# Kernel optimization log

Measured on AMD Instinct MI355X. Metric: run time of the kernel, lower is better.

## Reference

```python
import jax, jax.numpy as jnp
import numpy as np

N, E = 100000, 1600000
NODE_DIM, EDGE_DIM, HID = 128, 64, 128

def _mlp(x, w1, b1, w2, b2):
    # 2-layer MLP: Linear -> ReLU -> Linear (weights stored torch-style [out,in])
    return jax.nn.relu(x @ w1.T + b1) @ w2.T + b2

def setup_inputs() -> dict:
    key = jax.random.key(0)
    ks = jax.random.split(key, 24)
    g = lambda k, shp, fan: jax.random.normal(k, shp, jnp.float32) * (1.0 / np.sqrt(fan))
    return {
        "x": jax.random.normal(ks[0], (N, NODE_DIM), jnp.float32),
        "pos": jax.random.normal(ks[1], (N, 3), jnp.float32),
        "edge_index": jax.random.randint(ks[2], (2, E), 0, N),
        "edge_attr": jax.random.normal(ks[3], (E, EDGE_DIM), jnp.float32),
        # node_net: MLP(node_dim -> hid -> hid)
        "node_w1": g(ks[4], (HID, NODE_DIM), NODE_DIM), "node_b1": jnp.zeros((HID,), jnp.float32),
        "node_w2": g(ks[5], (HID, HID), HID), "node_b2": jnp.zeros((HID,), jnp.float32),
        # edge_net: MLP(edge_dim -> hid -> hid)
        "edge_w1": g(ks[6], (HID, EDGE_DIM), EDGE_DIM), "edge_b1": jnp.zeros((HID,), jnp.float32),
        "edge_w2": g(ks[7], (HID, HID), HID), "edge_b2": jnp.zeros((HID,), jnp.float32),
        # msg_net: Linear(hid, hid)
        "msg_w": g(ks[8], (HID, HID), HID), "msg_b": jnp.zeros((HID,), jnp.float32),
        # gate: MLP(edge_dim + node_dim -> hid -> hid)
        "gate_w1": g(ks[9], (HID, EDGE_DIM + NODE_DIM), EDGE_DIM + NODE_DIM), "gate_b1": jnp.zeros((HID,), jnp.float32),
        "gate_w2": g(ks[10], (HID, HID), HID), "gate_b2": jnp.zeros((HID,), jnp.float32),
        # centroid_lin: Linear(node_dim, hid)
        "cent_w": g(ks[11], (HID, NODE_DIM), NODE_DIM), "cent_b": jnp.zeros((HID,), jnp.float32),
        # layer norm
        "ln_g": jnp.ones((HID,), jnp.float32), "ln_b": jnp.zeros((HID,), jnp.float32),
        # out_transform: Linear(hid, node_dim)
        "out_w": g(ks[12], (NODE_DIM, HID), HID), "out_b": jnp.zeros((NODE_DIM,), jnp.float32),
    }

def reference(x, pos, edge_index, edge_attr,
              node_w1, node_b1, node_w2, node_b2,
              edge_w1, edge_b1, edge_w2, edge_b2,
              msg_w, msg_b,
              gate_w1, gate_b1, gate_w2, gate_b2,
              cent_w, cent_b, ln_g, ln_b, out_w, out_b):
    row, col = edge_index[0], edge_index[1]
    h_node = _mlp(x, node_w1, node_b1, node_w2, node_b2)          # (N, HID)
    h_edge = _mlp(edge_attr, edge_w1, edge_b1, edge_w2, edge_b2)   # (E, HID)
    msg_j = (h_edge * h_node[col]) @ msg_w.T + msg_b               # (E, HID)
    gate = _mlp(jnp.concatenate([edge_attr, x[col]], axis=-1),
                gate_w1, gate_b1, gate_w2, gate_b2)                # (E, HID)
    msg_j = msg_j * jax.nn.sigmoid(gate)
    aggr = jax.ops.segment_sum(msg_j, row, num_segments=x.shape[0])  # (N, HID)
    out = (x @ cent_w.T + cent_b) + aggr
    mu = jnp.mean(out, axis=-1, keepdims=True)
    var = jnp.var(out, axis=-1, keepdims=True)
    out = (out - mu) * jax.lax.rsqrt(var + 1e-5) * ln_g + ln_b
    return jax.nn.relu(out) @ out_w.T + out_b                      # (N, NODE_DIM)
```

## Files before the change

### kernel.cpp

```cpp
#include <hip/hip_runtime.h>

#define NN 100000
#define NE 1600000

typedef __bf16 bf16;
typedef bf16 bf16x8 __attribute__((ext_vector_type(8)));
typedef bf16 bf16x4 __attribute__((ext_vector_type(4)));
typedef float f32x4 __attribute__((ext_vector_type(4)));

__device__ __forceinline__ f32x4 mfma16(bf16x8 a, bf16x8 b, f32x4 c) {
    return __builtin_amdgcn_mfma_f32_16x16x32_bf16(a, b, c, 0, 0, 0);
}

__global__ void cvt_kernel(const float* __restrict__ s, bf16* __restrict__ d, int n4) {
    int i = blockIdx.x * 256 + threadIdx.x;
    if (i < n4) {
        f32x4 v = ((const f32x4*)s)[i];
        bf16x4 o;
        o[0] = (bf16)v[0]; o[1] = (bf16)v[1]; o[2] = (bf16)v[2]; o[3] = (bf16)v[3];
        ((bf16x4*)d)[i] = o;
    }
}

__launch_bounds__(256, 3)
__global__ void node_kernel(const bf16* __restrict__ xb,
                            const bf16* __restrict__ w1, const float* __restrict__ b1,
                            const bf16* __restrict__ w2, const float* __restrict__ b2,
                            const bf16* __restrict__ wc, const float* __restrict__ bc,
                            const bf16* __restrict__ wg1,
                            float* __restrict__ h_node, float* __restrict__ cent,
                            float* __restrict__ gx) {
    const int S = 136;
    __shared__ __align__(16) bf16 sX[64 * S];
    __shared__ __align__(16) bf16 sH[64 * S];
    const int tid = threadIdx.x;
    const int m0 = blockIdx.x * 64;
    {
        int e = tid >> 2, p = tid & 3;
        int gm = m0 + e;
        uint4 z = {0, 0, 0, 0};
        uint4* dst = (uint4*)(sX + e * S + p * 32);
        if (gm < NN) {
            const uint4* src = (const uint4*)(xb + (size_t)gm * 128 + p * 32);
#pragma unroll
            for (int j = 0; j < 4; ++j) dst[j] = src[j];
        } else {
#pragma unroll
            for (int j = 0; j < 4; ++j) dst[j] = z;
        }
    }
    __syncthreads();
    const int lane = tid & 63, wave = tid >> 6, t16 = lane & 15, quad = lane >> 4;
    const int n0 = wave * 32, koff = quad * 8;
    const f32x4 z4 = {0.f, 0.f, 0.f, 0.f};
    f32x4 acc[4][2];

#pragma unroll
    for (int mt = 0; mt < 4; ++mt) { acc[mt][0] = z4; acc[mt][1] = z4; }
#pragma unroll
    for (int ks = 0; ks < 4; ++ks) {
        bf16x8 bb0 = *(const bf16x8*)(w1 + (n0 + t16) * 128 + ks * 32 + koff);
        bf16x8 bb1 = *(const bf16x8*)(w1 + (n0 + 16 + t16) * 128 + ks * 32 + koff);
#pragma unroll
        for (int mt = 0; mt < 4; ++mt) {
            bf16x8 a = *(const bf16x8*)(sX + (mt * 16 + t16) * S + ks * 32 + koff);
            acc[mt][0] = mfma16(a, bb0, acc[mt][0]);
            acc[mt][1] = mfma16(a, bb1, acc[mt][1]);
        }
    }
    {
        float bi0 = b1[n0 + t16], bi1 = b1[n0 + 16 + t16];
#pragma unroll
        for (int mt = 0; mt < 4; ++mt)
#pragma unroll
            for (int nt = 0; nt < 2; ++nt) {
                int n = n0 + nt * 16 + t16;
                float bb = nt ? bi1 : bi0;
#pragma unroll
                for (int r = 0; r < 4; ++r) {
                    float v = acc[mt][nt][r] + bb;
                    sH[(mt * 16 + quad * 4 + r) * S + n] = (bf16)(v > 0.f ? v : 0.f);
                }
            }
    }
    __syncthreads();

#pragma unroll
    for (int mt = 0; mt < 4; ++mt) { acc[mt][0] = z4; acc[mt][1] = z4; }
#pragma unroll
    for (int ks = 0; ks < 4; ++ks) {
        bf16x8 bb0 = *(const bf16x8*)(w2 + (n0 + t16) * 128 + ks * 32 + koff);
        bf16x8 bb1 = *(const bf16x8*)(w2 + (n0 + 16 + t16) * 128 + ks * 32 + koff);
#pragma unroll
        for (int mt = 0; mt < 4; ++mt) {
            bf16x8 a = *(const bf16x8*)(sH + (mt * 16 + t16) * S + ks * 32 + koff);
            acc[mt][0] = mfma16(a, bb0, acc[mt][0]);
            acc[mt][1] = mfma16(a, bb1, acc[mt][1]);
        }
    }
    {
        float bi0 = b2[n0 + t16], bi1 = b2[n0 + 16 + t16];
#pragma unroll
        for (int mt = 0; mt < 4; ++mt)
#pragma unroll
            for (int nt = 0; nt < 2; ++nt) {
                int n = n0 + nt * 16 + t16;
                float bb = nt ? bi1 : bi0;
#pragma unroll
                for (int r = 0; r < 4; ++r) {
                    int gm = m0 + mt * 16 + quad * 4 + r;
                    if (gm < NN) h_node[(size_t)gm * 128 + n] = acc[mt][nt][r] + bb;
                }
            }
    }

#pragma unroll
    for (int mt = 0; mt < 4; ++mt) { acc[mt][0] = z4; acc[mt][1] = z4; }
#pragma unroll
    for (int ks = 0; ks < 4; ++ks) {
        bf16x8 bb0 = *(const bf16x8*)(wc + (n0 + t16) * 128 + ks * 32 + koff);
        bf16x8 bb1 = *(const bf16x8*)(wc + (n0 + 16 + t16) * 128 + ks * 32 + koff);
#pragma unroll
        for (int mt = 0; mt < 4; ++mt) {
            bf16x8 a = *(const bf16x8*)(sX + (mt * 16 + t16) * S + ks * 32 + koff);
            acc[mt][0] = mfma16(a, bb0, acc[mt][0]);
            acc[mt][1] = mfma16(a, bb1, acc[mt][1]);
        }
    }
    {
        float bi0 = bc[n0 + t16], bi1 = bc[n0 + 16 + t16];
#pragma unroll
        for (int mt = 0; mt < 4; ++mt)
#pragma unroll
            for (int nt = 0; nt < 2; ++nt) {
                int n = n0 + nt * 16 + t16;
                float bb = nt ? bi1 : bi0;
#pragma unroll
                for (int r = 0; r < 4; ++r) {
                    int gm = m0 + mt * 16 + quad * 4 + r;
                    if (gm < NN) cent[(size_t)gm * 128 + n] = acc[mt][nt][r] + bb;
                }
            }
    }

#pragma unroll
    for (int mt = 0; mt < 4; ++mt) { acc[mt][0] = z4; acc[mt][1] = z4; }
#pragma unroll
    for (int ks = 0; ks < 4; ++ks) {
        bf16x8 bb0 = *(const bf16x8*)(wg1 + (n0 + t16) * 192 + 64 + ks * 32 + koff);
        bf16x8 bb1 = *(const bf16x8*)(wg1 + (n0 + 16 + t16) * 192 + 64 + ks * 32 + koff);
#pragma unroll
        for (int mt = 0; mt < 4; ++mt) {
            bf16x8 a = *(const bf16x8*)(sX + (mt * 16 + t16) * S + ks * 32 + koff);
            acc[mt][0] = mfma16(a, bb0, acc[mt][0]);
            acc[mt][1] = mfma16(a, bb1, acc[mt][1]);
        }
    }
#pragma unroll
    for (int mt = 0; mt < 4; ++mt)
#pragma unroll
        for (int nt = 0; nt < 2; ++nt) {
            int n = n0 + nt * 16 + t16;
#pragma unroll
            for (int r = 0; r < 4; ++r) {
                int gm = m0 + mt * 16 + quad * 4 + r;
                if (gm < NN) gx[(size_t)gm * 128 + n] = acc[mt][nt][r];
            }
        }
}

__launch_bounds__(256, 3)
__global__ void edge_kernel(const float* __restrict__ edge_attr,
                            const int* __restrict__ erow, const int* __restrict__ ecol,
                            const float* __restrict__ hnode, const float* __restrict__ gx,
                            const bf16* __restrict__ we1, const float* __restrict__ be1,
                            const bf16* __restrict__ we2, const float* __restrict__ be2,
                            const bf16* __restrict__ wm, const float* __restrict__ bm,
                            const bf16* __restrict__ wg1, const float* __restrict__ bg1,
                            const bf16* __restrict__ wg2, const float* __restrict__ bg2,
                            float* __restrict__ aggr) {
    const int SE = 72, S = 136;
    __shared__ __align__(16) bf16 sEA[64 * SE];
    __shared__ __align__(16) bf16 sT[64 * S];
    __shared__ __align__(16) bf16 sX[64 * S];
    __shared__ int rowS[64], colS[64];
    const int tid = threadIdx.x;
    const int e0 = blockIdx.x * 64;
    if (tid < 64) { rowS[tid] = erow[e0 + tid]; colS[tid] = ecol[e0 + tid]; }
#pragma unroll
    for (int i = 0; i < 4; ++i) {
        int idx = tid * 4 + i * 1024;
        int e = idx >> 6, k = idx & 63;
        f32x4 v = *(const f32x4*)(edge_attr + (size_t)(e0 + e) * 64 + k);
        bf16x4 o;
        o[0] = (bf16)v[0]; o[1] = (bf16)v[1]; o[2] = (bf16)v[2]; o[3] = (bf16)v[3];
        *(bf16x4*)(sEA + e * SE + k) = o;
    }
    __syncthreads();
    const int lane = tid & 63, wave = tid >> 6, t16 = lane & 15, quad = lane >> 4;
    const int n0 = wave * 32, koff = quad * 8;
    const f32x4 z4 = {0.f, 0.f, 0.f, 0.f};
    f32x4 acc[4][2];

    float gval[4][2][4];
#pragma unroll
    for (int mt = 0; mt < 4; ++mt)
#pragma unroll
        for (int r = 0; r < 4; ++r) {
            const float* grow = gx + (size_t)colS[mt * 16 + quad * 4 + r] * 128;
            gval[mt][0][r] = grow[n0 + t16];
            gval[mt][1][r] = grow[n0 + 16 + t16];
        }

#pragma unroll
    for (int mt = 0; mt < 4; ++mt) { acc[mt][0] = z4; acc[mt][1] = z4; }
#pragma unroll
    for (int ks = 0; ks < 2; ++ks) {
        bf16x8 bb0 = *(const bf16x8*)(wg1 + (n0 + t16) * 192 + ks * 32 + koff);
        bf16x8 bb1 = *(const bf16x8*)(wg1 + (n0 + 16 + t16) * 192 + ks * 32 + koff);
#pragma unroll
        for (int mt = 0; mt < 4; ++mt) {
            bf16x8 a = *(const bf16x8*)(sEA + (mt * 16 + t16) * SE + ks * 32 + koff);
            acc[mt][0] = mfma16(a, bb0, acc[mt][0]);
            acc[mt][1] = mfma16(a, bb1, acc[mt][1]);
        }
    }
    {
        float bi0 = bg1[n0 + t16], bi1 = bg1[n0 + 16 + t16];
#pragma unroll
        for (int mt = 0; mt < 4; ++mt)
#pragma unroll
            for (int nt = 0; nt < 2; ++nt) {
                int n = n0 + nt * 16 + t16;
                float bb = nt ? bi1 : bi0;
#pragma unroll
                for (int r = 0; r < 4; ++r) {
                    float v = acc[mt][nt][r] + bb + gval[mt][nt][r];
                    sT[(mt * 16 + quad * 4 + r) * S + n] = (bf16)(v > 0.f ? v : 0.f);
                }
            }
    }
    __syncthreads();

    f32x4 gsig[4][2];
#pragma unroll
    for (int mt = 0; mt < 4; ++mt) { gsig[mt][0] = z4; gsig[mt][1] = z4; acc[mt][0] = z4; acc[mt][1] = z4; }
#pragma unroll
    for (int ks = 0; ks < 4; ++ks) {
        bf16x8 bb0 = *(const bf16x8*)(wg2 + (n0 + t16) * 128 + ks * 32 + koff);
        bf16x8 bb1 = *(const bf16x8*)(wg2 + (n0 + 16 + t16) * 128 + ks * 32 + koff);
#pragma unroll
        for (int mt = 0; mt < 4; ++mt) {
            bf16x8 a = *(const bf16x8*)(sT + (mt * 16 + t16) * S + ks * 32 + koff);
            gsig[mt][0] = mfma16(a, bb0, gsig[mt][0]);
            gsig[mt][1] = mfma16(a, bb1, gsig[mt][1]);
        }
    }
#pragma unroll
    for (int ks = 0; ks < 2; ++ks) {
        bf16x8 bb0 = *(const bf16x8*)(we1 + (n0 + t16) * 64 + ks * 32 + koff);
        bf16x8 bb1 = *(const bf16x8*)(we1 + (n0 + 16 + t16) * 64 + ks * 32 + koff);
#pragma unroll
        for (int mt = 0; mt < 4; ++mt) {
            bf16x8 a = *(const bf16x8*)(sEA + (mt * 16 + t16) * SE + ks * 32 + koff);
            acc[mt][0] = mfma16(a, bb0, acc[mt][0]);
            acc[mt][1] = mfma16(a, bb1, acc[mt][1]);
        }
    }
    {
        float bi0 = bg2[n0 + t16], bi1 = bg2[n0 + 16 + t16];
#pragma unroll
        for (int mt = 0; mt < 4; ++mt)
#pragma unroll
            for (int nt = 0; nt < 2; ++nt) {
                float bb = nt ? bi1 : bi0;
#pragma unroll
                for (int r = 0; r < 4; ++r) {
                    float v = gsig[mt][nt][r] + bb;
                    gsig[mt][nt][r] = 1.f / (1.f + __expf(-v));
                }
            }
    }
    {
        float bi0 = be1[n0 + t16], bi1 = be1[n0 + 16 + t16];
#pragma unroll
        for (int mt = 0; mt < 4; ++mt)
#pragma unroll
            for (int nt = 0; nt < 2; ++nt) {
                int n = n0 + nt * 16 + t16;
                float bb = nt ? bi1 : bi0;
#pragma unroll
                for (int r = 0; r < 4; ++r) {
                    float v = acc[mt][nt][r] + bb;
                    sX[(mt * 16 + quad * 4 + r) * S + n] = (bf16)(v > 0.f ? v : 0.f);
                }
            }
    }
    __syncthreads();

    float hval[4][2][4];
#pragma unroll
    for (int mt = 0; mt < 4; ++mt)
#pragma unroll
        for (int r = 0; r < 4; ++r) {
            const float* h = hnode + (size_t)colS[mt * 16 + quad * 4 + r] * 128;
            hval[mt][0][r] = h[n0 + t16];
            hval[mt][1][r] = h[n0 + 16 + t16];
        }

#pragma unroll
    for (int mt = 0; mt < 4; ++mt) { acc[mt][0] = z4; acc[mt][1] = z4; }
#pragma unroll
    for (int ks = 0; ks < 4; ++ks) {
        bf16x8 bb0 = *(const bf16x8*)(we2 + (n0 + t16) * 128 + ks * 32 + koff);
        bf16x8 bb1 = *(const bf16x8*)(we2 + (n0 + 16 + t16) * 128 + ks * 32 + koff);
#pragma unroll
        for (int mt = 0; mt < 4; ++mt) {
            bf16x8 a = *(const bf16x8*)(sX + (mt * 16 + t16) * S + ks * 32 + koff);
            acc[mt][0] = mfma16(a, bb0, acc[mt][0]);
            acc[mt][1] = mfma16(a, bb1, acc[mt][1]);
        }
    }
    {
        float bi0 = be2[n0 + t16], bi1 = be2[n0 + 16 + t16];
#pragma unroll
        for (int mt = 0; mt < 4; ++mt)
#pragma unroll
            for (int nt = 0; nt < 2; ++nt) {
                float bb = nt ? bi1 : bi0;
#pragma unroll
                for (int r = 0; r < 4; ++r)
                    acc[mt][nt][r] = (acc[mt][nt][r] + bb) * hval[mt][nt][r];
            }
    }
    __syncthreads();

#pragma unroll
    for (int mt = 0; mt < 4; ++mt)
#pragma unroll
        for (int nt = 0; nt < 2; ++nt) {
            int n = n0 + nt * 16 + t16;
#pragma unroll
            for (int r = 0; r < 4; ++r) {
                float p = acc[mt][nt][r];
                bf16 hi = (bf16)p;
                sT[(mt * 16 + quad * 4 + r) * S + n] = hi;
                sX[(mt * 16 + quad * 4 + r) * S + n] = (bf16)(p - (float)hi);
            }
        }
    __syncthreads();

#pragma unroll
    for (int mt = 0; mt < 4; ++mt) { acc[mt][0] = z4; acc[mt][1] = z4; }
#pragma unroll
    for (int ks = 0; ks < 4; ++ks) {
        bf16x8 bb0 = *(const bf16x8*)(wm + (n0 + t16) * 128 + ks * 32 + koff);
        bf16x8 bb1 = *(const bf16x8*)(wm + (n0 + 16 + t16) * 128 + ks * 32 + koff);
#pragma unroll
        for (int mt = 0; mt < 4; ++mt) {
            bf16x8 ah = *(const bf16x8*)(sT + (mt * 16 + t16) * S + ks * 32 + koff);
            bf16x8 al = *(const bf16x8*)(sX + (mt * 16 + t16) * S + ks * 32 + koff);
            acc[mt][0] = mfma16(ah, bb0, acc[mt][0]);
            acc[mt][0] = mfma16(al, bb0, acc[mt][0]);
            acc[mt][1] = mfma16(ah, bb1, acc[mt][1]);
            acc[mt][1] = mfma16(al, bb1, acc[mt][1]);
        }
    }
    {
        float bi0 = bm[n0 + t16], bi1 = bm[n0 + 16 + t16];
#pragma unroll
        for (int mt = 0; mt < 4; ++mt)
#pragma unroll
            for (int nt = 0; nt < 2; ++nt) {
                int n = n0 + nt * 16 + t16;
                float bb = nt ? bi1 : bi0;
#pragma unroll
                for (int r = 0; r < 4; ++r) {
                    int mloc = mt * 16 + quad * 4 + r;
                    float v = (acc[mt][nt][r] + bb) * gsig[mt][nt][r];
                    atomicAdd(aggr + (size_t)rowS[mloc] * 128 + n, v);
                }
            }
    }
}

__launch_bounds__(256, 3)
__global__ void final_kernel(const float* __restrict__ cent, const float* __restrict__ aggr,
                             const float* __restrict__ lng, const float* __restrict__ lnb,
                             const bf16* __restrict__ wo, const float* __restrict__ bo,
                             float* __restrict__ out) {
    const int S = 136;
    __shared__ __align__(16) bf16 sA[128 * S];
    const int tid = threadIdx.x;
    const int m0 = blockIdx.x * 128;
    {
        int r = tid >> 1, h = tid & 1;
        int gm = m0 + r;
        f32x4 vb[16];
        float sum = 0.f, sq = 0.f;
        if (gm < NN) {
            const f32x4* c4 = (const f32x4*)(cent + (size_t)gm * 128 + h * 64);
            const f32x4* a4 = (const f32x4*)(aggr + (size_t)gm * 128 + h * 64);
#pragma unroll
            for (int j = 0; j < 16; ++j) {
                f32x4 v = c4[j] + a4[j];
                vb[j] = v;
                sum += v[0] + v[1] + v[2] + v[3];
                sq += v[0] * v[0] + v[1] * v[1] + v[2] * v[2] + v[3] * v[3];
            }
        } else {
            f32x4 z = {0.f, 0.f, 0.f, 0.f};
#pragma unroll
            for (int j = 0; j < 16; ++j) vb[j] = z;
        }
        sum += __shfl_xor(sum, 1);
        sq += __shfl_xor(sq, 1);
        float mu = sum * (1.f / 128.f);
        float var = sq * (1.f / 128.f) - mu * mu;
        float rs = rsqrtf(var + 1e-5f);
#pragma unroll
        for (int j = 0; j < 16; ++j) {
            bf16x4 o;
#pragma unroll
            for (int c = 0; c < 4; ++c) {
                int k = h * 64 + j * 4 + c;
                float y = (vb[j][c] - mu) * rs * lng[k] + lnb[k];
                y = y > 0.f ? y : 0.f;
                o[c] = (bf16)(gm < NN ? y : 0.f);
            }
            *(bf16x4*)(sA + r * S + h * 64 + j * 4) = o;
        }
    }
    __syncthreads();
    const int lane = tid & 63, wave = tid >> 6, t16 = lane & 15, quad = lane >> 4;
    const int n0 = wave * 32, koff = quad * 8;
    const f32x4 z4 = {0.f, 0.f, 0.f, 0.f};
    f32x4 acc[8][2];
#pragma unroll
    for (int mt = 0; mt < 8; ++mt) { acc[mt][0] = z4; acc[mt][1] = z4; }
#pragma unroll
    for (int ks = 0; ks < 4; ++ks) {
        bf16x8 bb0 = *(const bf16x8*)(wo + (n0 + t16) * 128 + ks * 32 + koff);
        bf16x8 bb1 = *(const bf16x8*)(wo + (n0 + 16 + t16) * 128 + ks * 32 + koff);
#pragma unroll
        for (int mt = 0; mt < 8; ++mt) {
            bf16x8 a = *(const bf16x8*)(sA + (mt * 16 + t16) * S + ks * 32 + koff);
            acc[mt][0] = mfma16(a, bb0, acc[mt][0]);
            acc[mt][1] = mfma16(a, bb1, acc[mt][1]);
        }
    }
    {
        float bi0 = bo[n0 + t16], bi1 = bo[n0 + 16 + t16];
#pragma unroll
        for (int mt = 0; mt < 8; ++mt)
#pragma unroll
            for (int nt = 0; nt < 2; ++nt) {
                int n = n0 + nt * 16 + t16;
                float bb = nt ? bi1 : bi0;
#pragma unroll
                for (int r = 0; r < 4; ++r) {
                    int gm = m0 + mt * 16 + quad * 4 + r;
                    if (gm < NN) out[(size_t)gm * 128 + n] = acc[mt][nt][r] + bb;
                }
            }
    }
}

extern "C" void kernel_launch(void* const* d_in, const int* in_sizes, int n_in,
                              void* d_out, int out_size, void* d_ws, size_t ws_size,
                              hipStream_t stream) {
    bf16* wsb = (bf16*)d_ws;
    bf16* nw1 = wsb + 0;
    bf16* nw2 = wsb + 16384;
    bf16* cw = wsb + 32768;
    bf16* ew1 = wsb + 49152;
    bf16* ew2 = wsb + 57344;
    bf16* mw = wsb + 73728;
    bf16* gw1 = wsb + 90112;
    bf16* gw2 = wsb + 114688;
    bf16* ow = wsb + 131072;
    bf16* xb = wsb + 147456;
    float* hb = (float*)(xb + (size_t)NN * 128);
    float* cent = hb + (size_t)NN * 128;
    float* aggr = cent + (size_t)NN * 128;
    float* gx = aggr + (size_t)NN * 128;

    auto cv = [&](int idx, bf16* dst, int n) {
        cvt_kernel<<<(n / 4 + 255) / 256, 256, 0, stream>>>((const float*)d_in[idx], dst, n / 4);
    };
    cv(4, nw1, 16384);
    cv(6, nw2, 16384);
    cv(18, cw, 16384);
    cv(8, ew1, 8192);
    cv(10, ew2, 16384);
    cv(12, mw, 16384);
    cv(14, gw1, 24576);
    cv(16, gw2, 16384);
    cv(22, ow, 16384);
    cv(0, xb, NN * 128);
    hipMemsetAsync(aggr, 0, (size_t)NN * 128 * sizeof(float), stream);

    node_kernel<<<(NN + 63) / 64, 256, 0, stream>>>(
        xb, nw1, (const float*)d_in[5], nw2, (const float*)d_in[7],
        cw, (const float*)d_in[19], gw1, hb, cent, gx);

    const int* ei = (const int*)d_in[2];
    edge_kernel<<<NE / 64, 256, 0, stream>>>(
        (const float*)d_in[3], ei, ei + NE, hb, gx,
        ew1, (const float*)d_in[9], ew2, (const float*)d_in[11],
        mw, (const float*)d_in[13], gw1, (const float*)d_in[15],
        gw2, (const float*)d_in[17], aggr);

    final_kernel<<<(NN + 127) / 128, 256, 0, stream>>>(
        cent, aggr, (const float*)d_in[20], (const float*)d_in[21],
        ow, (const float*)d_in[23], (float*)d_out);
}
```

Measured before the change: 1.419 ms.

## Use fixed-point int64 atomics for aggregation and split-bf16 edge layer two

Aggregation now uses 64-bit fixed-point integer atomics instead of float atomics, so the sum no longer depends on the order of the adds. The centroid term is written straight into the integer accumulator, which removes the separate cent buffer and the memset. The conversion of x to bf16 is folded into the node kernel. The second edge-MLP layer now runs a hi/lo split-bf16 GEMM for accuracy, doubling its MFMA count. Each atomic is now 64-bit and the aggregation buffer is twice as large, which adds memory traffic and atomic cost. The edge kernel also gains an extra barrier.

```diff
diff --git a/kernel.cpp b/kernel.cpp
--- a/kernel.cpp
+++ b/kernel.cpp
@@ -7,6 +7,10 @@
 typedef bf16 bf16x8 __attribute__((ext_vector_type(8)));
 typedef bf16 bf16x4 __attribute__((ext_vector_type(4)));
 typedef float f32x4 __attribute__((ext_vector_type(4)));
+typedef long long ll;
+
+#define AGG_SCALE 1048576.0f
+#define AGG_INV   (1.0f / 1048576.0f)
 
 __device__ __forceinline__ f32x4 mfma16(bf16x8 a, bf16x8 b, f32x4 c) {
     return __builtin_amdgcn_mfma_f32_16x16x32_bf16(a, b, c, 0, 0, 0);
@@ -23,12 +27,12 @@
 }
 
 __launch_bounds__(256, 3)
-__global__ void node_kernel(const bf16* __restrict__ xb,
+__global__ void node_kernel(const float* __restrict__ x,
                             const bf16* __restrict__ w1, const float* __restrict__ b1,
                             const bf16* __restrict__ w2, const float* __restrict__ b2,
                             const bf16* __restrict__ wc, const float* __restrict__ bc,
                             const bf16* __restrict__ wg1,
-                            float* __restrict__ h_node, float* __restrict__ cent,
+                            float* __restrict__ h_node, ll* __restrict__ aggi,
                             float* __restrict__ gx) {
     const int S = 136;
     __shared__ __align__(16) bf16 sX[64 * S];
@@ -38,15 +42,19 @@
     {
         int e = tid >> 2, p = tid & 3;
         int gm = m0 + e;
-        uint4 z = {0, 0, 0, 0};
-        uint4* dst = (uint4*)(sX + e * S + p * 32);
         if (gm < NN) {
-            const uint4* src = (const uint4*)(xb + (size_t)gm * 128 + p * 32);
-#pragma unroll
-            for (int j = 0; j < 4; ++j) dst[j] = src[j];
+            const f32x4* src = (const f32x4*)(x + (size_t)gm * 128 + p * 32);
+#pragma unroll
+            for (int j = 0; j < 8; ++j) {
+                f32x4 v = src[j];
+                bf16x4 o;
+                o[0] = (bf16)v[0]; o[1] = (bf16)v[1]; o[2] = (bf16)v[2]; o[3] = (bf16)v[3];
+                *(bf16x4*)(sX + e * S + p * 32 + j * 4) = o;
+            }
         } else {
-#pragma unroll
-            for (int j = 0; j < 4; ++j) dst[j] = z;
+            uint2 z = {0, 0};
+#pragma unroll
+            for (int j = 0; j < 8; ++j) *(uint2*)(sX + e * S + p * 32 + j * 4) = z;
         }
     }
     __syncthreads();
@@ -138,7 +146,8 @@
 #pragma unroll
                 for (int r = 0; r < 4; ++r) {
                     int gm = m0 + mt * 16 + quad * 4 + r;
-                    if (gm < NN) cent[(size_t)gm * 128 + n] = acc[mt][nt][r] + bb;
+                    if (gm < NN)
+                        aggi[(size_t)gm * 128 + n] = llrintf((acc[mt][nt][r] + bb) * AGG_SCALE);
                 }
             }
     }
@@ -178,7 +187,7 @@
                             const bf16* __restrict__ wm, const float* __restrict__ bm,
                             const bf16* __restrict__ wg1, const float* __restrict__ bg1,
                             const bf16* __restrict__ wg2, const float* __restrict__ bg2,
-                            float* __restrict__ aggr) {
+                            ll* __restrict__ aggi) {
     const int SE = 72, S = 136;
     __shared__ __align__(16) bf16 sEA[64 * SE];
     __shared__ __align__(16) bf16 sT[64 * S];
@@ -281,6 +290,8 @@
                 }
             }
     }
+    __syncthreads();
+
     {
         float bi0 = be1[n0 + t16], bi1 = be1[n0 + 16 + t16];
 #pragma unroll
@@ -292,7 +303,11 @@
 #pragma unroll
                 for (int r = 0; r < 4; ++r) {
                     float v = acc[mt][nt][r] + bb;
-                    sX[(mt * 16 + quad * 4 + r) * S + n] = (bf16)(v > 0.f ? v : 0.f);
+                    v = v > 0.f ? v : 0.f;
+                    bf16 hi = (bf16)v;
+                    int idx = (mt * 16 + quad * 4 + r) * S + n;
+                    sX[idx] = hi;
+                    sT[idx] = (bf16)(v - (float)hi);
                 }
             }
     }
@@ -316,9 +331,12 @@
         bf16x8 bb1 = *(const bf16x8*)(we2 + (n0 + 16 + t16) * 128 + ks * 32 + koff);
 #pragma unroll
         for (int mt = 0; mt < 4; ++mt) {
-            bf16x8 a = *(const bf16x8*)(sX + (mt * 16 + t16) * S + ks * 32 + koff);
-            acc[mt][0] = mfma16(a, bb0, acc[mt][0]);
-            acc[mt][1] = mfma16(a, bb1, acc[mt][1]);
+            bf16x8 ahi = *(const bf16x8*)(sX + (mt * 16 + t16) * S + ks * 32 + koff);
+            bf16x8 alo = *(const bf16x8*)(sT + (mt * 16 + t16) * S + ks * 32 + koff);
+            acc[mt][0] = mfma16(ahi, bb0, acc[mt][0]);
+            acc[mt][0] = mfma16(alo, bb0, acc[mt][0]);
+            acc[mt][1] = mfma16(ahi, bb1, acc[mt][1]);
+            acc[mt][1] = mfma16(alo, bb1, acc[mt][1]);
         }
     }
     {
@@ -344,8 +362,9 @@
             for (int r = 0; r < 4; ++r) {
                 float p = acc[mt][nt][r];
                 bf16 hi = (bf16)p;
-                sT[(mt * 16 + quad * 4 + r) * S + n] = hi;
-                sX[(mt * 16 + quad * 4 + r) * S + n] = (bf16)(p - (float)hi);
+                int idx = (mt * 16 + quad * 4 + r) * S + n;
+                sT[idx] = hi;
+                sX[idx] = (bf16)(p - (float)hi);
             }
         }
     __syncthreads();
@@ -378,14 +397,16 @@
                 for (int r = 0; r < 4; ++r) {
                     int mloc = mt * 16 + quad * 4 + r;
                     float v = (acc[mt][nt][r] + bb) * gsig[mt][nt][r];
-                    atomicAdd(aggr + (size_t)rowS[mloc] * 128 + n, v);
+                    ll q = llrintf(v * AGG_SCALE);
+                    atomicAdd((unsigned long long*)(aggi + (size_t)rowS[mloc] * 128 + n),
+                              (unsigned long long)q);
                 }
             }
     }
 }
 
 __launch_bounds__(256, 3)
-__global__ void final_kernel(const float* __restrict__ cent, const float* __restrict__ aggr,
+__global__ void final_kernel(const ll* __restrict__ aggi,
                              const float* __restrict__ lng, const float* __restrict__ lnb,
                              const bf16* __restrict__ wo, const float* __restrict__ bo,
                              float* __restrict__ out) {
@@ -399,11 +420,15 @@
         f32x4 vb[16];
         float sum = 0.f, sq = 0.f;
         if (gm < NN) {
-            const f32x4* c4 = (const f32x4*)(cent + (size_t)gm * 128 + h * 64);
-            const f32x4* a4 = (const f32x4*)(aggr + (size_t)gm * 128 + h * 64);
+            const longlong2* a2 = (const longlong2*)(aggi + (size_t)gm * 128 + h * 64);
 #pragma unroll
             for (int j = 0; j < 16; ++j) {
-                f32x4 v = c4[j] + a4[j];
+                longlong2 p0 = a2[2 * j], p1 = a2[2 * j + 1];
+                f32x4 v;
+                v[0] = (float)p0.x * AGG_INV;
+                v[1] = (float)p0.y * AGG_INV;
+                v[2] = (float)p1.x * AGG_INV;
+                v[3] = (float)p1.y * AGG_INV;
                 vb[j] = v;
                 sum += v[0] + v[1] + v[2] + v[3];
                 sq += v[0] * v[0] + v[1] * v[1] + v[2] * v[2] + v[3] * v[3];
@@ -479,11 +504,9 @@
     bf16* gw1 = wsb + 90112;
     bf16* gw2 = wsb + 114688;
     bf16* ow = wsb + 131072;
-    bf16* xb = wsb + 147456;
-    float* hb = (float*)(xb + (size_t)NN * 128);
-    float* cent = hb + (size_t)NN * 128;
-    float* aggr = cent + (size_t)NN * 128;
-    float* gx = aggr + (size_t)NN * 128;
+    float* hb = (float*)(wsb + 147456);
+    float* gx = hb + (size_t)NN * 128;
+    ll* aggi = (ll*)(gx + (size_t)NN * 128);
 
     auto cv = [&](int idx, bf16* dst, int n) {
         cvt_kernel<<<(n / 4 + 255) / 256, 256, 0, stream>>>((const float*)d_in[idx], dst, n / 4);
@@ -497,21 +520,19 @@
     cv(14, gw1, 24576);
     cv(16, gw2, 16384);
     cv(22, ow, 16384);
-    cv(0, xb, NN * 128);
-    hipMemsetAsync(aggr, 0, (size_t)NN * 128 * sizeof(float), stream);
 
     node_kernel<<<(NN + 63) / 64, 256, 0, stream>>>(
-        xb, nw1, (const float*)d_in[5], nw2, (const float*)d_in[7],
-        cw, (const float*)d_in[19], gw1, hb, cent, gx);
+        (const float*)d_in[0], nw1, (const float*)d_in[5], nw2, (const float*)d_in[7],
+        cw, (const float*)d_in[19], gw1, hb, aggi, gx);
 
     const int* ei = (const int*)d_in[2];
     edge_kernel<<<NE / 64, 256, 0, stream>>>(
         (const float*)d_in[3], ei, ei + NE, hb, gx,
         ew1, (const float*)d_in[9], ew2, (const float*)d_in[11],
         mw, (const float*)d_in[13], gw1, (const float*)d_in[15],
-        gw2, (const float*)d_in[17], aggr);
+        gw2, (const float*)d_in[17], aggi);
 
     final_kernel<<<(NN + 127) / 128, 256, 0, stream>>>(
-        cent, aggr, (const float*)d_in[20], (const float*)d_in[21],
+        aggi, (const float*)d_in[20], (const float*)d_in[21],
         ow, (const float*)d_in[23], (float*)d_out);
 }
```

Result: slower. 1.787 ms (+25.9%).
